# Kernel optimization log

Measured on AMD Instinct MI355X. Metric: run time of the kernel, lower is better.

The kernel has to match this reference:

```python
import jax, jax.numpy as jnp
import numpy as np

N_STREAMS = 4
TAU = 1.0
ALPHA = 0.1
CAYLEY_ITERS = 2
LN_EPS = 1e-5


def setup_inputs() -> dict:
    key = jax.random.key(0)
    k1, k2, k3 = jax.random.split(key, 3)
    b, l, d = 2, 4096, 2048
    n = N_STREAMS
    x = jax.random.normal(k1, (b, l, d), dtype=jnp.float32)
    ln_w = jnp.ones((d,), dtype=jnp.float32)
    ln_b = jnp.zeros((d,), dtype=jnp.float32)
    # CastedLinear: trunc_normal std = 1/sqrt(in_features)
    proj_w = jax.random.truncated_normal(k2, -2.0, 2.0, (3 * n * n, d), dtype=jnp.float32) / jnp.sqrt(d * 1.0)
    proj_b = jnp.zeros((3 * n * n,), dtype=jnp.float32)
    # sublayer_fn realized as a dense linear (typical transformer sublayer core)
    W_sub = jax.random.normal(k3, (d, d), dtype=jnp.float32) / jnp.sqrt(d * 1.0)
    return {"x": x, "ln_w": ln_w, "ln_b": ln_b, "proj_w": proj_w, "proj_b": proj_b, "W_sub": W_sub}


def _layernorm(x, w, b):
    mu = jnp.mean(x, axis=-1, keepdims=True)
    var = jnp.mean(jnp.square(x - mu), axis=-1, keepdims=True)
    return (x - mu) * jax.lax.rsqrt(var + LN_EPS) * w + b


def _iterative_cayley(raw):
    # raw: (b, l, n, n) fp32
    w = raw - jnp.swapaxes(raw, -1, -2)
    eye = jnp.eye(N_STREAMS, dtype=raw.dtype)
    y = eye + ALPHA * w
    for _ in range(CAYLEY_ITERS):
        y = eye + 0.5 * ALPHA * jnp.matmul(w, eye + y)
    return y


def reference(x, ln_w, ln_b, proj_w, proj_b, W_sub):
    b, l, d = x.shape
    n = N_STREAMS
    gates = _layernorm(x, ln_w, ln_b) @ proj_w.T + proj_b  # (b, l, 3*n*n)
    pre_raw, post_raw, res_raw = jnp.split(gates, 3, axis=-1)
    pre_raw = pre_raw.reshape(b, l, n, n).astype(jnp.float32)
    post_raw = post_raw.reshape(b, l, n, n).astype(jnp.float32)
    res_raw = res_raw.reshape(b, l, n, n).astype(jnp.float32)
    h_pre = jax.nn.softmax(pre_raw / TAU, axis=-1)
    h_post = jax.nn.softmax(post_raw / TAU, axis=-2)
    h_res = _iterative_cayley(res_raw)
    # All streams of x_streams are identical copies of x, so
    # einsum('blij,bljd->blid', h, x_streams).mean(-2) == mean_i(sum_j h[i,j]) * x.
    coeff_pre = jnp.mean(jnp.sum(h_pre, axis=-1), axis=-1)    # (b, l)
    coeff_res = jnp.mean(jnp.sum(h_res, axis=-1), axis=-1)    # (b, l)
    coeff_post = jnp.mean(jnp.sum(h_post, axis=-1), axis=-1)  # (b, l)
    x_in = coeff_pre[..., None] * x
    y = x_in @ W_sub  # sublayer_fn
    return coeff_res[..., None] * x + coeff_post[..., None] * y
```

## Files before the change

### kernel.cpp

```cpp
#include <hip/hip_runtime.h>
#include <stdint.h>


typedef __attribute__((ext_vector_type(8))) __bf16 bf16x8;
typedef __attribute__((ext_vector_type(4))) float f32x4;
typedef __attribute__((ext_vector_type(8))) unsigned short us8;
typedef __attribute__((ext_vector_type(4))) unsigned short us4;

__device__ __forceinline__ unsigned short f2bf(float f) {
  union { float f; unsigned int u; } v; v.f = f;
  unsigned int u = v.u;
  u += 0x7fffu + ((u >> 16) & 1u);
  return (unsigned short)(u >> 16);
}

__device__ __forceinline__ float bf2f(unsigned short u) {
  union { unsigned int u; float f; } v; v.u = (unsigned int)u << 16;
  return v.f;
}

__device__ __forceinline__ void gload_lds16(const void* g, void* l) {
  __builtin_amdgcn_global_load_lds(
      (__attribute__((address_space(1))) void*)g,
      (__attribute__((address_space(3))) void*)l, 16, 0, 0);
}

__global__ __launch_bounds__(256) void k_ln_conv(
    const float* __restrict__ x, const float* __restrict__ lw, const float* __restrict__ lb,
    unsigned short* __restrict__ xb, unsigned short* __restrict__ lnb, int D) {
  const int t = blockIdx.x;
  const int tid = threadIdx.x;
  const float* row = x + (size_t)t * D;
  f32x4 a = *(const f32x4*)(row + tid * 8);
  f32x4 b = *(const f32x4*)(row + tid * 8 + 4);
  float vv[8] = {a[0], a[1], a[2], a[3], b[0], b[1], b[2], b[3]};
  float s = 0.f, ss = 0.f;
#pragma unroll
  for (int j = 0; j < 8; ++j) { s += vv[j]; ss += vv[j] * vv[j]; }
#pragma unroll
  for (int off = 32; off > 0; off >>= 1) { s += __shfl_down(s, off); ss += __shfl_down(ss, off); }
  __shared__ float red[8];
  __shared__ float st[2];
  int lane = tid & 63, wv = tid >> 6;
  if (lane == 0) { red[wv] = s; red[4 + wv] = ss; }
  __syncthreads();
  if (tid == 0) {
    float S = red[0] + red[1] + red[2] + red[3];
    float SS = red[4] + red[5] + red[6] + red[7];
    float mu = S / (float)D;
    float var = SS / (float)D - mu * mu;
    st[0] = mu; st[1] = rsqrtf(var + 1e-5f);
  }
  __syncthreads();
  float mu = st[0], rstd = st[1];
  f32x4 w0 = *(const f32x4*)(lw + tid * 8), w1 = *(const f32x4*)(lw + tid * 8 + 4);
  f32x4 b0 = *(const f32x4*)(lb + tid * 8), b1 = *(const f32x4*)(lb + tid * 8 + 4);
  float ww[8] = {w0[0], w0[1], w0[2], w0[3], w1[0], w1[1], w1[2], w1[3]};
  float bb[8] = {b0[0], b0[1], b0[2], b0[3], b1[0], b1[1], b1[2], b1[3]};
  us8 ox, ol;
#pragma unroll
  for (int j = 0; j < 8; ++j) {
    ox[j] = f2bf(vv[j]);
    ol[j] = f2bf((vv[j] - mu) * rstd * ww[j] + bb[j]);
  }
  *(us8*)(xb + (size_t)t * D + tid * 8) = ox;
  *(us8*)(lnb + (size_t)t * D + tid * 8) = ol;
}

__global__ __launch_bounds__(256) void k_wt(const float* __restrict__ W,
                                            unsigned short* __restrict__ Wt, int D) {
  __shared__ float tile[64][65];
  int kb = blockIdx.x * 64, nb = blockIdx.y * 64;
  int tid = threadIdx.x;
  int tx = tid & 15, ty = tid >> 4;
#pragma unroll
  for (int p = 0; p < 4; ++p) {
    int r = p * 16 + ty;
    f32x4 v = *(const f32x4*)(W + (size_t)(kb + r) * D + nb + tx * 4);
    tile[r][tx * 4 + 0] = v[0]; tile[r][tx * 4 + 1] = v[1];
    tile[r][tx * 4 + 2] = v[2]; tile[r][tx * 4 + 3] = v[3];
  }
  __syncthreads();
#pragma unroll
  for (int p = 0; p < 2; ++p) {
    int c = p * 256 + tid;
    int nr = c >> 3, kc = (c & 7) * 8;
    us8 o;
#pragma unroll
    for (int j = 0; j < 8; ++j) o[j] = f2bf(tile[kc + j][nr]);
    *(us8*)(Wt + (size_t)(nb + nr) * D + kb + kc) = o;
  }
}

__global__ void k_pconv(const float* __restrict__ p, unsigned short* __restrict__ q, int n) {
  int i = (blockIdx.x * 256 + threadIdx.x) * 4;
  if (i < n) {
    f32x4 v = *(const f32x4*)(p + i);
    us4 o;
#pragma unroll
    for (int j = 0; j < 4; ++j) o[j] = f2bf(v[j]);
    *(us4*)(q + i) = o;
  }
}

__global__ __launch_bounds__(256) void k_gates(
    const unsigned short* __restrict__ A,
    const unsigned short* __restrict__ Bp,
    const float* __restrict__ pb,
    float* __restrict__ cresp, float* __restrict__ cpyp, int K) {
  __shared__ __attribute__((aligned(16))) unsigned short As[128 * 32];
  __shared__ __attribute__((aligned(16))) unsigned short Bs[48 * 32];
  __shared__ float gl[128][49];
  __shared__ float pbs[48];
  int tid = threadIdx.x, lane = tid & 63, wv = tid >> 6;
  if (tid < 48) pbs[tid] = pb[tid];
  f32x4 acc[2][3] = {};
  size_t rowBase = (size_t)blockIdx.x * 128;
  for (int k0 = 0; k0 < K; k0 += 32) {
#pragma unroll
    for (int inst = 0; inst < 2; ++inst) {
      int eo = inst * 2048 + wv * 512 + lane * 8;
      int r = eo >> 5, cc = eo & 31;
      gload_lds16(A + (rowBase + r) * K + k0 + cc, (char*)As + inst * 4096 + wv * 1024);
    }
    if (tid < 192) {
      int r = tid >> 2, cc = (tid & 3) * 8;
      us8 v = *(const us8*)(Bp + (size_t)r * K + k0 + cc);
      *(us8*)(Bs + r * 32 + cc) = v;
    }
    __syncthreads();
    int kb = (lane >> 4) * 8, rr = lane & 15;
    bf16x8 av[2], bv[3];
#pragma unroll
    for (int mi = 0; mi < 2; ++mi)
      av[mi] = *(const bf16x8*)(As + (wv * 32 + mi * 16 + rr) * 32 + kb);
#pragma unroll
    for (int ni = 0; ni < 3; ++ni)
      bv[ni] = *(const bf16x8*)(Bs + (ni * 16 + rr) * 32 + kb);
#pragma unroll
    for (int mi = 0; mi < 2; ++mi)
#pragma unroll
      for (int ni = 0; ni < 3; ++ni)
        acc[mi][ni] = __builtin_amdgcn_mfma_f32_16x16x32_bf16(av[mi], bv[ni], acc[mi][ni], 0, 0, 0);
    __syncthreads();
  }
#pragma unroll
  for (int mi = 0; mi < 2; ++mi)
#pragma unroll
    for (int ni = 0; ni < 3; ++ni)
#pragma unroll
      for (int i = 0; i < 4; ++i)
        gl[wv * 32 + mi * 16 + (lane >> 4) * 4 + i][ni * 16 + (lane & 15)] = acc[mi][ni][i];
  __syncthreads();
  if (tid < 128) {
    float g[48];
#pragma unroll
    for (int j = 0; j < 48; ++j) g[j] = gl[tid][j] + pbs[j];
    float cpre = 0.f;
#pragma unroll
    for (int i = 0; i < 4; ++i) {
      float m = fmaxf(fmaxf(g[i * 4], g[i * 4 + 1]), fmaxf(g[i * 4 + 2], g[i * 4 + 3]));
      float e0 = expf(g[i * 4] - m), e1 = expf(g[i * 4 + 1] - m);
      float e2 = expf(g[i * 4 + 2] - m), e3 = expf(g[i * 4 + 3] - m);
      float inv = 1.f / (e0 + e1 + e2 + e3);
      cpre += e0 * inv + e1 * inv + e2 * inv + e3 * inv;
    }
    cpre *= 0.25f;
    float cpost = 0.f;
#pragma unroll
    for (int j = 0; j < 4; ++j) {
      float a0 = g[16 + j], a1 = g[20 + j], a2 = g[24 + j], a3 = g[28 + j];
      float m = fmaxf(fmaxf(a0, a1), fmaxf(a2, a3));
      float e0 = expf(a0 - m), e1 = expf(a1 - m), e2 = expf(a2 - m), e3 = expf(a3 - m);
      float inv = 1.f / (e0 + e1 + e2 + e3);
      cpost += e0 * inv + e1 * inv + e2 * inv + e3 * inv;
    }
    cpost *= 0.25f;
    float w4[16], y4[16];
#pragma unroll
    for (int i = 0; i < 4; ++i)
#pragma unroll
      for (int j = 0; j < 4; ++j)
        w4[i * 4 + j] = g[32 + i * 4 + j] - g[32 + j * 4 + i];
#pragma unroll
    for (int i = 0; i < 16; ++i) y4[i] = 0.1f * w4[i];
    y4[0] += 1.f; y4[5] += 1.f; y4[10] += 1.f; y4[15] += 1.f;
#pragma unroll
    for (int it = 0; it < 2; ++it) {
      float z[16];
#pragma unroll
      for (int i = 0; i < 16; ++i) z[i] = y4[i];
      z[0] += 1.f; z[5] += 1.f; z[10] += 1.f; z[15] += 1.f;
#pragma unroll
      for (int i = 0; i < 4; ++i)
#pragma unroll
        for (int j = 0; j < 4; ++j) {
          float acc2 = 0.f;
#pragma unroll
          for (int k = 0; k < 4; ++k) acc2 += w4[i * 4 + k] * z[k * 4 + j];
          y4[i * 4 + j] = ((i == j) ? 1.f : 0.f) + 0.05f * acc2;
        }
    }
    float cr = 0.f;
#pragma unroll
    for (int i = 0; i < 16; ++i) cr += y4[i];
    cr *= 0.25f;
    cresp[rowBase + tid] = cr;
    cpyp[rowBase + tid] = cpre * cpost;
  }
}

__global__ __launch_bounds__(512, 2) void k_gemm(
    const unsigned short* __restrict__ A,
    const unsigned short* __restrict__ Bt,
    const unsigned short* __restrict__ xbr,
    const float* __restrict__ cresp, const float* __restrict__ cpyp,
    float* __restrict__ out, int M, int N, int K) {
  __shared__ __attribute__((aligned(16))) unsigned short As[4][256 * 32];
  __shared__ __attribute__((aligned(16))) unsigned short Bs[4][256 * 32];
  const int tid = threadIdx.x, lane = tid & 63, wv = tid >> 6;
  const int nbm = M >> 8;
  const int nwg = nbm * (N >> 8);
  const int chunk = nwg >> 3;
  const int gid = (blockIdx.x & 7) * chunk + (blockIdx.x >> 3);
  const int bn = gid / nbm, bm = gid % nbm;
  const int wm = wv >> 2, wn = wv & 3;
  const int rr = lane & 15, ksl = lane >> 4;
  const int koff = (ksl ^ ((rr >> 1) & 3)) * 8;
  const int rloc = tid >> 2;
  const int cbelem = ((tid & 3) ^ ((tid >> 3) & 3)) * 8;
  const unsigned short* aG = A + (size_t)((bm << 8) + rloc) * K + cbelem;
  const unsigned short* bG = Bt + (size_t)((bn << 8) + rloc) * K + cbelem;
  f32x4 acc[8][4] = {};
  const int nsl = K >> 5;

#define STAGE(KT, SLOT)                                                        \
  {                                                                            \
    const unsigned short* ag_ = aG + (KT) * 32;                                \
    const unsigned short* bg_ = bG + (KT) * 32;                                \
    unsigned short* la_ = &As[(SLOT)][wv * 512];                               \
    unsigned short* lb_ = &Bs[(SLOT)][wv * 512];                               \
    gload_lds16(ag_, la_);                                                     \
    gload_lds16(ag_ + (size_t)128 * K, la_ + 4096);                            \
    gload_lds16(bg_, lb_);                                                     \
    gload_lds16(bg_ + (size_t)128 * K, lb_ + 4096);                            \
  }

  STAGE(0, 0)
  STAGE(1, 1)
  STAGE(2, 2)

#define GBODY(S)                                                               \
  {                                                                            \
    asm volatile("s_waitcnt vmcnt(8)" ::: "memory");                           \
    __builtin_amdgcn_sched_barrier(0);                                         \
    __builtin_amdgcn_s_barrier();                                              \
    __builtin_amdgcn_sched_barrier(0);                                         \
    int kt_ = jb + (S) + 3;                                                    \
    if (kt_ > nsl - 1) kt_ = nsl - 1;                                          \
    STAGE(kt_, ((S) + 3) & 3)                                                  \
    __builtin_amdgcn_sched_barrier(0);                                         \
    const unsigned short* Ab = &As[(S)][(wm * 128 + rr) * 32 + koff];          \
    const unsigned short* Bb = &Bs[(S)][(wn * 64 + rr) * 32 + koff];           \
    bf16x8 av[8], bv[4];                                                       \
    _Pragma("unroll")                                                          \
    for (int mf = 0; mf < 8; ++mf) av[mf] = *(const bf16x8*)(Ab + mf * 512);   \
    _Pragma("unroll")                                                          \
    for (int nf = 0; nf < 4; ++nf) bv[nf] = *(const bf16x8*)(Bb + nf * 512);   \
    __builtin_amdgcn_s_setprio(1);                                             \
    _Pragma("unroll")                                                          \
    for (int mf = 0; mf < 8; ++mf)                                             \
      _Pragma("unroll")                                                        \
      for (int nf = 0; nf < 4; ++nf)                                           \
        acc[mf][nf] =                                                          \
            __builtin_amdgcn_mfma_f32_16x16x32_bf16(av[mf], bv[nf],            \
                                                    acc[mf][nf], 0, 0, 0);     \
    __builtin_amdgcn_s_setprio(0);                                             \
  }

  for (int jb = 0; jb < nsl; jb += 4) {
    GBODY(0)
    GBODY(1)
    GBODY(2)
    GBODY(3)
  }
#undef GBODY
#undef STAGE

  const int orow0 = (bm << 8) + wm * 128 + ksl * 4;
  const int ocol0 = (bn << 8) + wn * 64 + rr;
#pragma unroll
  for (int mf = 0; mf < 8; ++mf)
#pragma unroll
    for (int i = 0; i < 4; ++i) {
      const int row = orow0 + mf * 16 + i;
      const float crv = cresp[row], cpv = cpyp[row];
      const size_t base = (size_t)row * N + ocol0;
#pragma unroll
      for (int nf = 0; nf < 4; ++nf)
        out[base + nf * 16] = crv * bf2f(xbr[base + nf * 16]) + cpv * acc[mf][nf][i];
    }
}

extern "C" void kernel_launch(void* const* d_in, const int* in_sizes, int n_in,
                              void* d_out, int out_size, void* d_ws, size_t ws_size,
                              hipStream_t stream) {
  const float* x  = (const float*)d_in[0];
  const float* lw = (const float*)d_in[1];
  const float* lb = (const float*)d_in[2];
  const float* pw = (const float*)d_in[3];
  const float* pb = (const float*)d_in[4];
  const float* W  = (const float*)d_in[5];
  float* out = (float*)d_out;

  const int D = in_sizes[1];
  const int M = in_sizes[0] / D;
  const int G = in_sizes[4];

  char* ws = (char*)d_ws;
  size_t off = 0;
  unsigned short* xb  = (unsigned short*)(ws + off); off += (size_t)M * D * 2;
  unsigned short* lnb = (unsigned short*)(ws + off); off += (size_t)M * D * 2;
  unsigned short* Wt  = (unsigned short*)(ws + off); off += (size_t)D * D * 2;
  unsigned short* pjb = (unsigned short*)(ws + off); off += (size_t)G * D * 2;
  float* cres = (float*)(ws + off); off += (size_t)M * 4;
  float* cpy  = (float*)(ws + off); off += (size_t)M * 4;

  k_ln_conv<<<M, 256, 0, stream>>>(x, lw, lb, xb, lnb, D);
  k_wt<<<dim3(D / 64, D / 64), 256, 0, stream>>>(W, Wt, D);
  k_pconv<<<(G * D / 4 + 255) / 256, 256, 0, stream>>>(pw, pjb, G * D);
  k_gates<<<M / 128, 256, 0, stream>>>(lnb, pjb, pb, cres, cpy, D);

  const int nwg = (M / 256) * (D / 256);
  k_gemm<<<nwg, 512, 0, stream>>>(xb, Wt, xb, cres, cpy, out, M, D, D);
}
```

Before: 140.9 us.

## Fold LayerNorm into gate projection weights and correct in epilogue

Stops writing a separate bf16 LayerNorm output. The gate GEMM now reads the bf16 copy of x that is already produced, against projection weights prescaled by the LN weight. Per-row mean and rstd are applied afterwards in the gate epilogue, together with precomputed column sums of w*P and of P*b. This removes a 32 MB bf16 write and its later read, at the cost of a small extra kernel and some numerical risk, because the matmul now runs on unnormalized bf16 x and the mean is subtracted after accumulation.

```diff
diff --git a/kernel.cpp b/kernel.cpp
--- a/kernel.cpp
+++ b/kernel.cpp
@@ -25,9 +25,9 @@
       (__attribute__((address_space(3))) void*)l, 16, 0, 0);
 }
 
-__global__ __launch_bounds__(256) void k_ln_conv(
-    const float* __restrict__ x, const float* __restrict__ lw, const float* __restrict__ lb,
-    unsigned short* __restrict__ xb, unsigned short* __restrict__ lnb, int D) {
+__global__ __launch_bounds__(256) void k_lnx(
+    const float* __restrict__ x, unsigned short* __restrict__ xb,
+    float2* __restrict__ mur, int D) {
   const int t = blockIdx.x;
   const int tid = threadIdx.x;
   const float* row = x + (size_t)t * D;
@@ -40,7 +40,6 @@
 #pragma unroll
   for (int off = 32; off > 0; off >>= 1) { s += __shfl_down(s, off); ss += __shfl_down(ss, off); }
   __shared__ float red[8];
-  __shared__ float st[2];
   int lane = tid & 63, wv = tid >> 6;
   if (lane == 0) { red[wv] = s; red[4 + wv] = ss; }
   __syncthreads();
@@ -49,22 +48,13 @@
     float SS = red[4] + red[5] + red[6] + red[7];
     float mu = S / (float)D;
     float var = SS / (float)D - mu * mu;
-    st[0] = mu; st[1] = rsqrtf(var + 1e-5f);
-  }
-  __syncthreads();
-  float mu = st[0], rstd = st[1];
-  f32x4 w0 = *(const f32x4*)(lw + tid * 8), w1 = *(const f32x4*)(lw + tid * 8 + 4);
-  f32x4 b0 = *(const f32x4*)(lb + tid * 8), b1 = *(const f32x4*)(lb + tid * 8 + 4);
-  float ww[8] = {w0[0], w0[1], w0[2], w0[3], w1[0], w1[1], w1[2], w1[3]};
-  float bb[8] = {b0[0], b0[1], b0[2], b0[3], b1[0], b1[1], b1[2], b1[3]};
-  us8 ox, ol;
-#pragma unroll
-  for (int j = 0; j < 8; ++j) {
-    ox[j] = f2bf(vv[j]);
-    ol[j] = f2bf((vv[j] - mu) * rstd * ww[j] + bb[j]);
-  }
+    float2 o; o.x = mu; o.y = rsqrtf(var + 1e-5f);
+    mur[t] = o;
+  }
+  us8 ox;
+#pragma unroll
+  for (int j = 0; j < 8; ++j) ox[j] = f2bf(vv[j]);
   *(us8*)(xb + (size_t)t * D + tid * 8) = ox;
-  *(us8*)(lnb + (size_t)t * D + tid * 8) = ol;
 }
 
 __global__ __launch_bounds__(256) void k_wt(const float* __restrict__ W,
@@ -92,14 +82,34 @@
   }
 }
 
-__global__ void k_pconv(const float* __restrict__ p, unsigned short* __restrict__ q, int n) {
-  int i = (blockIdx.x * 256 + threadIdx.x) * 4;
-  if (i < n) {
-    f32x4 v = *(const f32x4*)(p + i);
+__global__ __launch_bounds__(256) void k_wp(
+    const float* __restrict__ P, const float* __restrict__ w, const float* __restrict__ b,
+    unsigned short* __restrict__ WPb, float* __restrict__ S, float* __restrict__ T, int K) {
+  const int j = blockIdx.x, tid = threadIdx.x;
+  float s = 0.f, t = 0.f;
+  for (int i = tid * 4; i < K; i += 1024) {
+    f32x4 pv = *(const f32x4*)(P + (size_t)j * K + i);
+    f32x4 wv = *(const f32x4*)(w + i);
+    f32x4 bv = *(const f32x4*)(b + i);
     us4 o;
 #pragma unroll
-    for (int j = 0; j < 4; ++j) o[j] = f2bf(v[j]);
-    *(us4*)(q + i) = o;
+    for (int q = 0; q < 4; ++q) {
+      float wp = pv[q] * wv[q];
+      o[q] = f2bf(wp);
+      s += wp;
+      t += pv[q] * bv[q];
+    }
+    *(us4*)(WPb + (size_t)j * K + i) = o;
+  }
+#pragma unroll
+  for (int off = 32; off > 0; off >>= 1) { s += __shfl_down(s, off); t += __shfl_down(t, off); }
+  __shared__ float rs[4], rt[4];
+  int lane = tid & 63, wvi = tid >> 6;
+  if (lane == 0) { rs[wvi] = s; rt[wvi] = t; }
+  __syncthreads();
+  if (tid == 0) {
+    S[j] = rs[0] + rs[1] + rs[2] + rs[3];
+    T[j] = rt[0] + rt[1] + rt[2] + rt[3];
   }
 }
 
@@ -107,13 +117,15 @@
     const unsigned short* __restrict__ A,
     const unsigned short* __restrict__ Bp,
     const float* __restrict__ pb,
+    const float2* __restrict__ mur,
+    const float* __restrict__ S, const float* __restrict__ T,
     float* __restrict__ cresp, float* __restrict__ cpyp, int K) {
   __shared__ __attribute__((aligned(16))) unsigned short As[128 * 32];
   __shared__ __attribute__((aligned(16))) unsigned short Bs[48 * 32];
   __shared__ float gl[128][49];
-  __shared__ float pbs[48];
+  __shared__ float pbs[48], Ss[48], Ts[48];
   int tid = threadIdx.x, lane = tid & 63, wv = tid >> 6;
-  if (tid < 48) pbs[tid] = pb[tid];
+  if (tid < 48) { pbs[tid] = pb[tid]; Ss[tid] = S[tid]; Ts[tid] = T[tid]; }
   f32x4 acc[2][3] = {};
   size_t rowBase = (size_t)blockIdx.x * 128;
   for (int k0 = 0; k0 < K; k0 += 32) {
@@ -153,9 +165,11 @@
         gl[wv * 32 + mi * 16 + (lane >> 4) * 4 + i][ni * 16 + (lane & 15)] = acc[mi][ni][i];
   __syncthreads();
   if (tid < 128) {
+    float2 mr = mur[rowBase + tid];
+    const float rmu = mr.y * mr.x;
     float g[48];
 #pragma unroll
-    for (int j = 0; j < 48; ++j) g[j] = gl[tid][j] + pbs[j];
+    for (int j = 0; j < 48; ++j) g[j] = mr.y * gl[tid][j] - rmu * Ss[j] + Ts[j] + pbs[j];
     float cpre = 0.f;
 #pragma unroll
     for (int i = 0; i < 4; ++i) {
@@ -320,16 +334,18 @@
   char* ws = (char*)d_ws;
   size_t off = 0;
   unsigned short* xb  = (unsigned short*)(ws + off); off += (size_t)M * D * 2;
-  unsigned short* lnb = (unsigned short*)(ws + off); off += (size_t)M * D * 2;
   unsigned short* Wt  = (unsigned short*)(ws + off); off += (size_t)D * D * 2;
-  unsigned short* pjb = (unsigned short*)(ws + off); off += (size_t)G * D * 2;
+  unsigned short* WPb = (unsigned short*)(ws + off); off += (size_t)G * D * 2;
+  float2* mur = (float2*)(ws + off); off += (size_t)M * 8;
+  float* Sv   = (float*)(ws + off); off += 64 * 4;
+  float* Tv   = (float*)(ws + off); off += 64 * 4;
   float* cres = (float*)(ws + off); off += (size_t)M * 4;
   float* cpy  = (float*)(ws + off); off += (size_t)M * 4;
 
-  k_ln_conv<<<M, 256, 0, stream>>>(x, lw, lb, xb, lnb, D);
+  k_lnx<<<M, 256, 0, stream>>>(x, xb, mur, D);
   k_wt<<<dim3(D / 64, D / 64), 256, 0, stream>>>(W, Wt, D);
-  k_pconv<<<(G * D / 4 + 255) / 256, 256, 0, stream>>>(pw, pjb, G * D);
-  k_gates<<<M / 128, 256, 0, stream>>>(lnb, pjb, pb, cres, cpy, D);
+  k_wp<<<G, 256, 0, stream>>>(pw, lw, lb, WPb, Sv, Tv, D);
+  k_gates<<<M / 128, 256, 0, stream>>>(xb, WPb, pb, mur, Sv, Tv, cres, cpy, D);
 
   const int nwg = (M / 256) * (D / 256);
   k_gemm<<<nwg, 512, 0, stream>>>(xb, Wt, xb, cres, cpy, out, M, D, D);
```

Result: faster. 133.2 us (-5.5%).
